# Kernel tuning notes

Hardware: AMD Instinct MI355X
Metric: run time of the kernel (lower is better)

Reference implementation:

```python
import jax, jax.numpy as jnp
import numpy as np

N_ENS = 4        # number of FGL sub-layers
B, N_IN, N_OUT = 1, 16384, 4096
IN_C, OUT_C = 16, 16
DENSITY = 0.10   # sparsity proxy for A + dA random perturbation


def setup_inputs() -> dict:
    key = jax.random.key(0)
    kx, ka, km, kw, kb = jax.random.split(key, 5)
    x = jax.random.normal(kx, (B, N_IN, IN_C), dtype=jnp.float32)
    # Dense storage of the n perturbed sparse adjacencies A_i (n_out, n_in)
    A_vals = jax.random.normal(ka, (N_ENS, N_OUT, N_IN), dtype=jnp.float32)
    A_mask = jax.random.bernoulli(km, DENSITY, (N_ENS, N_OUT, N_IN))
    As = A_vals * A_mask.astype(jnp.float32)
    Ws = jax.random.normal(kw, (N_ENS, IN_C, OUT_C), dtype=jnp.float32) * (1.0 / np.sqrt(IN_C))
    bs = jax.random.normal(kb, (N_ENS, OUT_C), dtype=jnp.float32) * 0.01
    return {"x": x, "As": As, "Ws": Ws, "bs": bs}


def reference(x, As, Ws, bs):
    # Each FGL_i: y_i = (A_i @ x) @ W_i + b_i
    # x: [b, n_in, f]; As: [n, n_out, n_in]; Ws: [n, f, g]; bs: [n, g]
    h = jnp.einsum('noi,bif->nbof', As, x)            # graph aggregation per ensemble member
    y = jnp.einsum('nbof,nfg->nbog', h, Ws)           # per-member linear transform
    y = y + bs[:, None, None, :]
    return jnp.mean(y, axis=0)                        # sum over n members / n
```

## Files before the change

kernel.cpp:

```cpp
#include <hip/hip_runtime.h>


#define N_ENS 4
#define N_OUT 4096
#define N_IN  16384
#define ROWS  (N_ENS * N_OUT)
#define GSPLIT 16
#define ICHUNK (N_IN / GSPLIT)
#define SROUND 256
#define NROUND (ICHUNK / SROUND)
#define NSTEP  (SROUND / 4)

__global__ __launch_bounds__(256) void k_transpose(const float* __restrict__ x,
                                                   float* __restrict__ xT) {
    int idx = blockIdx.x * 256 + threadIdx.x;
    int i = idx >> 4;
    int f = idx & 15;
    xT[f * N_IN + i] = x[idx];
}

__global__ __launch_bounds__(256, 4) void k_main(const float* __restrict__ A,
                                                 const float* __restrict__ xT,
                                                 float* __restrict__ h) {
    __shared__ float xs[2][16][SROUND];

    const int rb   = blockIdx.x & 63;
    const int g    = blockIdx.x >> 6;
    const int tid  = threadIdx.x;
    const int wave = tid >> 6;
    const int lane = tid & 63;
    const int o_sub = lane & 15;
    const int f_sub = lane >> 4;
    const int i0 = g * ICHUNK;
    const int rowbase = rb * 256 + wave * 64 + o_sub;

    const float* Arow = A + (size_t)rowbase * N_IN + i0;

    float acc[4][4];
#pragma unroll
    for (int k = 0; k < 4; ++k)
#pragma unroll
        for (int j = 0; j < 4; ++j) acc[k][j] = 0.0f;

    float4 pf[4];
    const int stg_f[4] = {wave, 4 + wave, 8 + wave, 12 + wave};

    auto stage_load = [&](int r) {
        const int ibase = i0 + r * SROUND;
#pragma unroll
        for (int c = 0; c < 4; ++c) {
            int f = stg_f[c];
            pf[c] = *(const float4*)(xT + (size_t)f * N_IN + ibase + (lane << 2));
        }
    };
    auto stage_write = [&](int buf) {
#pragma unroll
        for (int c = 0; c < 4; ++c) {
            int f = stg_f[c];
            int s = f >> 2;
            *(float4*)&xs[buf][f][(lane ^ s) << 2] = pf[c];
        }
    };

    stage_load(0);
    stage_write(0);
    __syncthreads();

    int buf = 0;
    for (int r = 0; r < NROUND; ++r) {
        if (r + 1 < NROUND) stage_load(r + 1);

        const float* Ap = Arow + r * SROUND;
#pragma unroll 4
        for (int q = 0; q < NSTEP; ++q) {
            float4 a[4];
#pragma unroll
            for (int k = 0; k < 4; ++k)
                a[k] = *(const float4*)(Ap + (size_t)k * 16 * N_IN + (q << 2));
            float4 xv[4];
#pragma unroll
            for (int j = 0; j < 4; ++j)
                xv[j] = *(const float4*)&xs[buf][f_sub * 4 + j][(q ^ f_sub) << 2];
#pragma unroll
            for (int k = 0; k < 4; ++k) {
#pragma unroll
                for (int j = 0; j < 4; ++j) {
                    acc[k][j] = fmaf(a[k].x, xv[j].x, acc[k][j]);
                    acc[k][j] = fmaf(a[k].y, xv[j].y, acc[k][j]);
                    acc[k][j] = fmaf(a[k].z, xv[j].z, acc[k][j]);
                    acc[k][j] = fmaf(a[k].w, xv[j].w, acc[k][j]);
                }
            }
        }

        if (r + 1 < NROUND) stage_write(buf ^ 1);
        __syncthreads();
        buf ^= 1;
    }

#pragma unroll
    for (int k = 0; k < 4; ++k) {
        int row = rowbase + 16 * k;
#pragma unroll
        for (int j = 0; j < 4; ++j)
            atomicAdd(&h[(size_t)row * 16 + f_sub * 4 + j], acc[k][j]);
    }
}

__global__ __launch_bounds__(256) void k_out(const float* __restrict__ h,
                                             const float* __restrict__ Ws,
                                             const float* __restrict__ bs,
                                             float* __restrict__ out) {
    __shared__ float Wsm[N_ENS * 16 * 16];
    __shared__ float bsm[N_ENS * 16];
    int tid = threadIdx.x;
#pragma unroll
    for (int r = 0; r < 4; ++r) Wsm[tid + 256 * r] = Ws[tid + 256 * r];
    if (tid < 64) bsm[tid] = bs[tid];
    __syncthreads();

    int idx = blockIdx.x * 256 + tid;
    int o = idx >> 4;
    int gg = idx & 15;
    float s = 0.0f;
#pragma unroll
    for (int n = 0; n < N_ENS; ++n) {
        const float* hr = h + ((size_t)(n * N_OUT + o) << 4);
        float t = 0.0f;
#pragma unroll
        for (int f = 0; f < 16; ++f)
            t = fmaf(hr[f], Wsm[n * 256 + f * 16 + gg], t);
        s += t + bsm[n * 16 + gg];
    }
    out[idx] = 0.25f * s;
}

extern "C" void kernel_launch(void* const* d_in, const int* in_sizes, int n_in,
                              void* d_out, int out_size, void* d_ws, size_t ws_size,
                              hipStream_t stream) {
    const float* x  = (const float*)d_in[0];
    const float* As = (const float*)d_in[1];
    const float* Ws = (const float*)d_in[2];
    const float* bs = (const float*)d_in[3];
    float* out = (float*)d_out;

    float* h  = (float*)d_ws;
    float* xT = (float*)((char*)d_ws + (1 << 20));

    hipMemsetAsync(h, 0, (size_t)ROWS * 16 * sizeof(float), stream);
    k_transpose<<<(N_IN * 16) / 256, 256, 0, stream>>>(x, xT);
    k_main<<<64 * GSPLIT, 256, 0, stream>>>(As, xT, h);
    k_out<<<(N_OUT * 16) / 256, 256, 0, stream>>>(h, Ws, bs, out);
}
```

Baseline: 1.622 ms.

## Replace LDS-staged tiled kernel with row-per-thread streaming and split partial sums

The main kernel now gives each thread one whole output row over a split of the input dimension. It streams 64 contiguous bytes of A per step and reads x directly with wave-uniform addresses, so the transpose kernel, the LDS double buffering and the barriers are gone. The atomicAdd reduction and the memset are replaced by per-split partial outputs in workspace, summed by a new k_hsum kernel. The split count doubles and the occupancy hint rises. The cost is per-lane strided A accesses that do not coalesce across lanes, plus a 32 MB partial-sum buffer that must be written and read back.

```diff
diff --git a/kernel.cpp b/kernel.cpp
--- a/kernel.cpp
+++ b/kernel.cpp
@@ -5,106 +5,54 @@
 #define N_OUT 4096
 #define N_IN  16384
 #define ROWS  (N_ENS * N_OUT)
-#define GSPLIT 16
+#define GSPLIT 32
 #define ICHUNK (N_IN / GSPLIT)
-#define SROUND 256
-#define NROUND (ICHUNK / SROUND)
-#define NSTEP  (SROUND / 4)
 
-__global__ __launch_bounds__(256) void k_transpose(const float* __restrict__ x,
-                                                   float* __restrict__ xT) {
-    int idx = blockIdx.x * 256 + threadIdx.x;
-    int i = idx >> 4;
-    int f = idx & 15;
-    xT[f * N_IN + i] = x[idx];
+__global__ __launch_bounds__(256, 6) void k_main(const float* __restrict__ A,
+                                                 const float* __restrict__ x,
+                                                 float* __restrict__ hp) {
+    const int split  = blockIdx.x & (GSPLIT - 1);
+    const int rowblk = blockIdx.x >> 5;
+    const int row = rowblk * 256 + threadIdx.x;
+    const int i0 = split * ICHUNK;
+
+    const float* Ap  = A + (size_t)row * N_IN + i0;
+    const float* xp0 = x + (size_t)i0 * 16;
+
+    float acc[16];
+#pragma unroll
+    for (int f = 0; f < 16; ++f) acc[f] = 0.0f;
+
+    for (int s = 0; s < ICHUNK / 16; ++s) {
+        float4 av4[4];
+#pragma unroll
+        for (int q = 0; q < 4; ++q)
+            av4[q] = *(const float4*)(Ap + s * 16 + q * 4);
+        const float* af = (const float*)av4;
+        const float* xp = xp0 + (size_t)s * 256;
+
+#pragma unroll
+        for (int ii = 0; ii < 16; ++ii) {
+            const float av = af[ii];
+#pragma unroll
+            for (int f = 0; f < 16; ++f)
+                acc[f] = fmaf(av, xp[ii * 16 + f], acc[f]);
+        }
+    }
+
+    float* outp = hp + ((size_t)split * ROWS + row) * 16;
+#pragma unroll
+    for (int f = 0; f < 16; ++f) outp[f] = acc[f];
 }
 
-__global__ __launch_bounds__(256, 4) void k_main(const float* __restrict__ A,
-                                                 const float* __restrict__ xT,
-                                                 float* __restrict__ h) {
-    __shared__ float xs[2][16][SROUND];
-
-    const int rb   = blockIdx.x & 63;
-    const int g    = blockIdx.x >> 6;
-    const int tid  = threadIdx.x;
-    const int wave = tid >> 6;
-    const int lane = tid & 63;
-    const int o_sub = lane & 15;
-    const int f_sub = lane >> 4;
-    const int i0 = g * ICHUNK;
-    const int rowbase = rb * 256 + wave * 64 + o_sub;
-
-    const float* Arow = A + (size_t)rowbase * N_IN + i0;
-
-    float acc[4][4];
+__global__ __launch_bounds__(256) void k_hsum(const float* __restrict__ hp,
+                                              float* __restrict__ h) {
+    int t = blockIdx.x * 256 + threadIdx.x;
+    float s = 0.0f;
 #pragma unroll
-    for (int k = 0; k < 4; ++k)
-#pragma unroll
-        for (int j = 0; j < 4; ++j) acc[k][j] = 0.0f;
-
-    float4 pf[4];
-    const int stg_f[4] = {wave, 4 + wave, 8 + wave, 12 + wave};
-
-    auto stage_load = [&](int r) {
-        const int ibase = i0 + r * SROUND;
-#pragma unroll
-        for (int c = 0; c < 4; ++c) {
-            int f = stg_f[c];
-            pf[c] = *(const float4*)(xT + (size_t)f * N_IN + ibase + (lane << 2));
-        }
-    };
-    auto stage_write = [&](int buf) {
-#pragma unroll
-        for (int c = 0; c < 4; ++c) {
-            int f = stg_f[c];
-            int s = f >> 2;
-            *(float4*)&xs[buf][f][(lane ^ s) << 2] = pf[c];
-        }
-    };
-
-    stage_load(0);
-    stage_write(0);
-    __syncthreads();
-
-    int buf = 0;
-    for (int r = 0; r < NROUND; ++r) {
-        if (r + 1 < NROUND) stage_load(r + 1);
-
-        const float* Ap = Arow + r * SROUND;
-#pragma unroll 4
-        for (int q = 0; q < NSTEP; ++q) {
-            float4 a[4];
-#pragma unroll
-            for (int k = 0; k < 4; ++k)
-                a[k] = *(const float4*)(Ap + (size_t)k * 16 * N_IN + (q << 2));
-            float4 xv[4];
-#pragma unroll
-            for (int j = 0; j < 4; ++j)
-                xv[j] = *(const float4*)&xs[buf][f_sub * 4 + j][(q ^ f_sub) << 2];
-#pragma unroll
-            for (int k = 0; k < 4; ++k) {
-#pragma unroll
-                for (int j = 0; j < 4; ++j) {
-                    acc[k][j] = fmaf(a[k].x, xv[j].x, acc[k][j]);
-                    acc[k][j] = fmaf(a[k].y, xv[j].y, acc[k][j]);
-                    acc[k][j] = fmaf(a[k].z, xv[j].z, acc[k][j]);
-                    acc[k][j] = fmaf(a[k].w, xv[j].w, acc[k][j]);
-                }
-            }
-        }
-
-        if (r + 1 < NROUND) stage_write(buf ^ 1);
-        __syncthreads();
-        buf ^= 1;
-    }
-
-#pragma unroll
-    for (int k = 0; k < 4; ++k) {
-        int row = rowbase + 16 * k;
-#pragma unroll
-        for (int j = 0; j < 4; ++j)
-            atomicAdd(&h[(size_t)row * 16 + f_sub * 4 + j], acc[k][j]);
-    }
+    for (int sp = 0; sp < GSPLIT; ++sp)
+        s += hp[(size_t)sp * (ROWS * 16) + t];
+    h[t] = s;
 }
 
 __global__ __launch_bounds__(256) void k_out(const float* __restrict__ h,
@@ -144,11 +92,10 @@
     const float* bs = (const float*)d_in[3];
     float* out = (float*)d_out;
 
-    float* h  = (float*)d_ws;
-    float* xT = (float*)((char*)d_ws + (1 << 20));
+    float* hp = (float*)d_ws;
+    float* h  = (float*)((char*)d_ws + (size_t)32 * 1024 * 1024);
 
-    hipMemsetAsync(h, 0, (size_t)ROWS * 16 * sizeof(float), stream);
-    k_transpose<<<(N_IN * 16) / 256, 256, 0, stream>>>(x, xT);
-    k_main<<<64 * GSPLIT, 256, 0, stream>>>(As, xT, h);
+    k_main<<<64 * GSPLIT, 256, 0, stream>>>(As, x, hp);
+    k_hsum<<<(ROWS * 16) / 256, 256, 0, stream>>>(hp, h);
     k_out<<<(N_OUT * 16) / 256, 256, 0, stream>>>(h, Ws, bs, out);
 }
```

New measurement: 1.415 ms. 12.7% less time.
